# Performance work log

Measured on AMD Instinct MI355X. Metric: run time of the kernel, lower is better.

Reference implementation:

```python
import jax, jax.numpy as jnp
import numpy as np


def _fwht(x):
    """Fast Walsh-Hadamard transform along the last axis (length must be 2^k)."""
    orig_shape = x.shape
    n = orig_shape[-1]
    x = x.reshape(-1, n)
    h = 1
    while h < n:
        # split last dim into (n // (2h), 2, h) blocks and do the butterfly
        x = x.reshape(-1, n // (2 * h), 2, h)
        a = x[:, :, 0, :]
        b = x[:, :, 1, :]
        x = jnp.stack([a + b, a - b], axis=2).reshape(-1, n)
        h *= 2
    return x.reshape(orig_shape)


def setup_inputs() -> dict:
    key = jax.random.key(0)
    x = jax.random.normal(key, (16384, 4096), dtype=jnp.float32)
    scale = jnp.ones((), dtype=jnp.float32)
    return {"x": x, "scale": scale}


def reference(x, scale):
    # Faithful to fwht(input, scale): Hadamard butterfly then scalar scale.
    return _fwht(x) * scale
```

## Files before the change

### kernel.cpp

```cpp
#include <hip/hip_runtime.h>


__device__ __forceinline__ void bfly(float& a, float& b) {
  const float x = a, y = b;
  a = x + y;
  b = x - y;
}

__global__ __launch_bounds__(256, 8) void fwht_kernel(
    const float* __restrict__ x, const float* __restrict__ scale,
    float* __restrict__ out) {
  __shared__ __align__(16) float lds[4348];
  const int t = threadIdx.x;
  const int row = blockIdx.x;
  const float* xr = x + (size_t)row * 4096;
  float* outr = out + (size_t)row * 4096;
  const float s = scale[0];

  float r[16];

#pragma unroll
  for (int k = 0; k < 4; ++k) {
    const float4 f = *reinterpret_cast<const float4*>(xr + k * 1024 + 4 * t);
    r[k * 4 + 0] = f.x; r[k * 4 + 1] = f.y;
    r[k * 4 + 2] = f.z; r[k * 4 + 3] = f.w;
  }

#pragma unroll
  for (int k = 0; k < 4; ++k) {
    bfly(r[k * 4 + 0], r[k * 4 + 1]); bfly(r[k * 4 + 2], r[k * 4 + 3]);
    bfly(r[k * 4 + 0], r[k * 4 + 2]); bfly(r[k * 4 + 1], r[k * 4 + 3]);
  }
#pragma unroll
  for (int c = 0; c < 4; ++c) {
    bfly(r[0 + c], r[4 + c]); bfly(r[8 + c], r[12 + c]);
    bfly(r[0 + c], r[8 + c]); bfly(r[4 + c], r[12 + c]);
  }

  {
    const int wb = 4 * t + 4 * (t >> 4);
#pragma unroll
    for (int k = 0; k < 4; ++k) {
      *reinterpret_cast<float4*>(&lds[k * 1088 + wb]) =
          make_float4(r[k * 4 + 0], r[k * 4 + 1], r[k * 4 + 2], r[k * 4 + 3]);
    }
  }
  __syncthreads();

  const int rb1 = (t >> 2) * 68 + (t & 3);
#pragma unroll
  for (int m = 0; m < 16; ++m) r[m] = lds[rb1 + 4 * m];

#pragma unroll
  for (int bit = 0; bit < 4; ++bit) {
    const int mask = 1 << bit;
#pragma unroll
    for (int m = 0; m < 16; ++m)
      if (!(m & mask)) bfly(r[m], r[m | mask]);
  }

#pragma unroll
  for (int m = 0; m < 16; ++m) lds[rb1 + 4 * m] = r[m];
  __syncthreads();

  const int rb2 = (t >> 6) * 1088 + (t & 63);
#pragma unroll
  for (int g = 0; g < 16; ++g) r[g] = lds[rb2 + 68 * g];

#pragma unroll
  for (int bit = 0; bit < 4; ++bit) {
    const int mask = 1 << bit;
#pragma unroll
    for (int g = 0; g < 16; ++g)
      if (!(g & mask)) bfly(r[g], r[g | mask]);
  }

  float* op = outr + (t >> 6) * 1024 + (t & 63);
#pragma unroll
  for (int g = 0; g < 16; ++g) op[g * 64] = r[g] * s;
}

extern "C" void kernel_launch(void* const* d_in, const int* in_sizes, int n_in,
                              void* d_out, int out_size, void* d_ws, size_t ws_size,
                              hipStream_t stream) {
  (void)in_sizes; (void)n_in; (void)d_ws; (void)ws_size; (void)out_size;
  const float* x = (const float*)d_in[0];
  const float* scale = (const float*)d_in[1];
  float* out = (float*)d_out;
  fwht_kernel<<<16384, 256, 0, stream>>>(x, scale, out);
}
```

Before: 425.8 us.

## Vectorize LDS and global accesses using DPP quad swaps for butterflies

The second and third transform stages are redistributed so each thread owns four float4 chunks. Two of the four butterfly bits in each stage are done across lanes of a quad with DPP quad_perm moves and sign-selected FMAs. This turns the scalar LDS reads and writes and the scalar global stores into 128-bit accesses, cutting instruction count and memory transactions. The cost is extra DPP and FMA instructions and a more intricate index mapping, which could break correctness if the permutation is wrong.

```diff
diff --git a/kernel.cpp b/kernel.cpp
--- a/kernel.cpp
+++ b/kernel.cpp
@@ -3,8 +3,13 @@
 
 __device__ __forceinline__ void bfly(float& a, float& b) {
   const float x = a, y = b;
-  a = x + y;
-  b = x - y;
+  a = x + y; b = x - y;
+}
+
+template <int CTRL>
+__device__ __forceinline__ float qswap(float v) {
+  return __int_as_float(
+      __builtin_amdgcn_mov_dpp(__float_as_int(v), CTRL, 0xF, 0xF, true));
 }
 
 __global__ __launch_bounds__(256, 8) void fwht_kernel(
@@ -16,6 +21,9 @@
   const float* xr = x + (size_t)row * 4096;
   float* outr = out + (size_t)row * 4096;
   const float s = scale[0];
+
+  const float sg1 = (t & 1) ? -1.0f : 1.0f;
+  const float sg2 = (t & 2) ? -1.0f : 1.0f;
 
   float r[16];
 
@@ -47,37 +55,56 @@
   }
   __syncthreads();
 
-  const int rb1 = (t >> 2) * 68 + (t & 3);
+  const int rb1 = 4 * (t & 3) + 68 * ((t >> 2) & 15) + 1088 * (t >> 6);
 #pragma unroll
-  for (int m = 0; m < 16; ++m) r[m] = lds[rb1 + 4 * m];
-
-#pragma unroll
-  for (int bit = 0; bit < 4; ++bit) {
-    const int mask = 1 << bit;
-#pragma unroll
-    for (int m = 0; m < 16; ++m)
-      if (!(m & mask)) bfly(r[m], r[m | mask]);
+  for (int q = 0; q < 4; ++q) {
+    const float4 f = *reinterpret_cast<const float4*>(&lds[rb1 + 16 * q]);
+    r[q * 4 + 0] = f.x; r[q * 4 + 1] = f.y;
+    r[q * 4 + 2] = f.z; r[q * 4 + 3] = f.w;
   }
 
 #pragma unroll
-  for (int m = 0; m < 16; ++m) lds[rb1 + 4 * m] = r[m];
+  for (int c = 0; c < 4; ++c) {
+    bfly(r[0 + c], r[4 + c]); bfly(r[8 + c], r[12 + c]);
+    bfly(r[0 + c], r[8 + c]); bfly(r[4 + c], r[12 + c]);
+  }
+#pragma unroll
+  for (int i = 0; i < 16; ++i) r[i] = fmaf(sg1, r[i], qswap<0xB1>(r[i]));
+#pragma unroll
+  for (int i = 0; i < 16; ++i) r[i] = fmaf(sg2, r[i], qswap<0x4E>(r[i]));
+
+#pragma unroll
+  for (int q = 0; q < 4; ++q) {
+    *reinterpret_cast<float4*>(&lds[rb1 + 16 * q]) =
+        make_float4(r[q * 4 + 0], r[q * 4 + 1], r[q * 4 + 2], r[q * 4 + 3]);
+  }
   __syncthreads();
 
-  const int rb2 = (t >> 6) * 1088 + (t & 63);
+  const int rb2 = 4 * ((t >> 2) & 15) + 68 * (t & 3) + 1088 * (t >> 6);
 #pragma unroll
-  for (int g = 0; g < 16; ++g) r[g] = lds[rb2 + 68 * g];
+  for (int q = 0; q < 4; ++q) {
+    const float4 f = *reinterpret_cast<const float4*>(&lds[rb2 + 272 * q]);
+    r[q * 4 + 0] = f.x; r[q * 4 + 1] = f.y;
+    r[q * 4 + 2] = f.z; r[q * 4 + 3] = f.w;
+  }
 
 #pragma unroll
-  for (int bit = 0; bit < 4; ++bit) {
-    const int mask = 1 << bit;
+  for (int c = 0; c < 4; ++c) {
+    bfly(r[0 + c], r[4 + c]); bfly(r[8 + c], r[12 + c]);
+    bfly(r[0 + c], r[8 + c]); bfly(r[4 + c], r[12 + c]);
+  }
 #pragma unroll
-    for (int g = 0; g < 16; ++g)
-      if (!(g & mask)) bfly(r[g], r[g | mask]);
+  for (int i = 0; i < 16; ++i) r[i] = fmaf(sg1, r[i], qswap<0xB1>(r[i]));
+#pragma unroll
+  for (int i = 0; i < 16; ++i) r[i] = fmaf(sg2, r[i], qswap<0x4E>(r[i]));
+
+  float* ob = outr + 4 * ((t >> 2) & 15) + 64 * (t & 3) + 1024 * (t >> 6);
+#pragma unroll
+  for (int q = 0; q < 4; ++q) {
+    *reinterpret_cast<float4*>(ob + 256 * q) =
+        make_float4(r[q * 4 + 0] * s, r[q * 4 + 1] * s,
+                    r[q * 4 + 2] * s, r[q * 4 + 3] * s);
   }
-
-  float* op = outr + (t >> 6) * 1024 + (t & 63);
-#pragma unroll
-  for (int g = 0; g < 16; ++g) op[g * 64] = r[g] * s;
 }
 
 extern "C" void kernel_launch(void* const* d_in, const int* in_sizes, int n_in,
```

After: 431.6 us. Within noise of the previous version (+1.4%).
